# Kernel optimization log

Measured on AMD Instinct MI355X. Metric: run time of the kernel, lower is better.

The kernel has to match this reference:

```python
import jax, jax.numpy as jnp
import numpy as np


def setup_inputs() -> dict:
    key = jax.random.key(0)
    k1, k2, k3 = jax.random.split(key, 3)
    B, N, F_in, F_out = 8, 2048, 128, 128
    x = jax.random.normal(k1, (B, N, F_in), dtype=jnp.float32)
    adj = jax.random.uniform(k2, (B, N, N), dtype=jnp.float32)
    W = jax.random.normal(k3, (F_out, F_in), dtype=jnp.float32) * (1.0 / np.sqrt(F_in))
    b = jnp.zeros((F_out,), dtype=jnp.float32)
    return {"x": x, "adj": adj, "W": W, "b": b}


def reference(x, adj, W, b):
    # adj: [B,N,N], x: [B,N,F]
    N = adj.shape[-1]
    adj = adj + jnp.eye(N, dtype=adj.dtype)  # add self-loops
    d_inv_sqrt = jnp.sum(adj, axis=-1) ** -0.5  # [B,N]
    # D^-1/2 A D^-1/2 as row/col broadcast scale (same math as diag bmm)
    adj_norm = d_inv_sqrt[:, :, None] * adj * d_inv_sqrt[:, None, :]
    out = jnp.einsum('bnm,bmf->bnf', adj_norm, x)  # aggregate
    out = jnp.einsum('bnf,of->bno', out, W) + b    # linear
    return out
```

## Files before the change

kernel.cpp:

```cpp
#include <hip/hip_runtime.h>
#include <hip/hip_bf16.h>

typedef __attribute__((ext_vector_type(8))) short s16x8;
typedef __attribute__((ext_vector_type(4))) float f32x4;

#define B_  8
#define N_  2048
#define F_  128
#define BM  64
#define BK  64

__device__ __forceinline__ short bfc(float f) {
  __hip_bfloat16 h = __float2bfloat16(f);
  return __builtin_bit_cast(short, h);
}

__global__ __launch_bounds__(256) void k_deg(const float* __restrict__ adj,
                                             float* __restrict__ dinv) {
  const int row  = blockIdx.x * 4 + (threadIdx.x >> 6);
  const int lane = threadIdx.x & 63;
  const float* p = adj + (size_t)row * N_;
  float s = 0.f;
#pragma unroll
  for (int it = 0; it < 8; ++it) {
    float4 v = *reinterpret_cast<const float4*>(p + it * 256 + lane * 4);
    s += (v.x + v.y) + (v.z + v.w);
  }
#pragma unroll
  for (int off = 32; off > 0; off >>= 1) s += __shfl_down(s, off);
  if (lane == 0) dinv[row] = 1.0f / sqrtf(s + 1.0f);
}

__global__ __launch_bounds__(512) void k_gcn(const float* __restrict__ adj,
                                             const float* __restrict__ x,
                                             const float* __restrict__ W,
                                             const float* __restrict__ bias,
                                             const float* __restrict__ dinv,
                                             float* __restrict__ out) {
  __shared__ short s_mem[BM * 72 + F_ * 72];
  __shared__ short s_w[F_ * 136];
  short* const s_adj = s_mem;
  short* const s_xb  = s_mem + BM * 72;
  short* const s_o1  = s_mem;

  const int tid  = threadIdx.x;
  const int lane = tid & 63;
  const int wv   = tid >> 6;
  const int wrow = wv & 3;
  const int whal = wv >> 2;

  const int batch = blockIdx.x & 7;
  const int n0    = (blockIdx.x >> 3) * BM;

  {
    const int o  = tid >> 2;
    const int f0 = (tid & 3) * 32;
    const float* wp = W + o * F_ + f0;
#pragma unroll
    for (int u = 0; u < 8; ++u) {
      float4 v = *reinterpret_cast<const float4*>(wp + u * 4);
      short4 h;
      h.x = bfc(v.x); h.y = bfc(v.y); h.z = bfc(v.z); h.w = bfc(v.w);
      *reinterpret_cast<short4*>(&s_w[o * 136 + f0 + u * 4]) = h;
    }
  }

  const int ai  = tid >> 3;
  const int aj  = (tid & 7) * 8;
  const int xk2 = tid >> 4;
  const int xf0 = (tid & 15) * 8;

  const float* adj_row = adj + (size_t)(batch * N_ + n0 + ai) * N_;
  const float* x_b     = x + (size_t)batch * N_ * F_;
  const float* dv_b    = dinv + batch * N_;

  float4 ra0, ra1, rx0, rx1, rx2, rx3;
  float rd0, rd1;

  auto issue = [&](int k0) {
    ra0 = *reinterpret_cast<const float4*>(adj_row + k0 + aj);
    ra1 = *reinterpret_cast<const float4*>(adj_row + k0 + aj + 4);
    const float* xr = x_b + (size_t)(k0 + 2 * xk2) * F_ + xf0;
    rx0 = *reinterpret_cast<const float4*>(xr);
    rx1 = *reinterpret_cast<const float4*>(xr + 4);
    rx2 = *reinterpret_cast<const float4*>(xr + F_);
    rx3 = *reinterpret_cast<const float4*>(xr + F_ + 4);
    rd0 = dv_b[k0 + 2 * xk2];
    rd1 = dv_b[k0 + 2 * xk2 + 1];
  };

  f32x4 acc[4] = {};

  issue(0);
#pragma unroll 1
  for (int t = 0; t < N_ / BK; ++t) {
    __syncthreads();
    {
      s16x8 h;
      h[0] = bfc(ra0.x); h[1] = bfc(ra0.y); h[2] = bfc(ra0.z); h[3] = bfc(ra0.w);
      h[4] = bfc(ra1.x); h[5] = bfc(ra1.y); h[6] = bfc(ra1.z); h[7] = bfc(ra1.w);
      *reinterpret_cast<s16x8*>(&s_adj[ai * 72 + aj]) = h;
    }
    {
      float a0[8] = {rx0.x, rx0.y, rx0.z, rx0.w, rx1.x, rx1.y, rx1.z, rx1.w};
      float a1[8] = {rx2.x, rx2.y, rx2.z, rx2.w, rx3.x, rx3.y, rx3.z, rx3.w};
      const int kbase = (2 * xk2) ^ ((tid & 7) << 3);
#pragma unroll
      for (int u = 0; u < 8; ++u) {
        unsigned lo = (unsigned short)bfc(a0[u] * rd0);
        unsigned hi = (unsigned short)bfc(a1[u] * rd1);
        *reinterpret_cast<unsigned*>(&s_xb[(xf0 + u) * 72 + kbase]) = lo | (hi << 16);
      }
    }
    if (t + 1 < N_ / BK) issue((t + 1) * BK);
    __syncthreads();
    {
      const int arow = (wrow * 16 + (lane & 15)) * 72 + ((lane >> 4) * 8);
      s16x8 a0 = *reinterpret_cast<const s16x8*>(&s_adj[arow]);
      s16x8 a1 = *reinterpret_cast<const s16x8*>(&s_adj[arow + 32]);
      const int krun = (lane >> 4) * 8;
#pragma unroll
      for (int ct = 0; ct < 4; ++ct) {
        const int f   = whal * 64 + ct * 16 + (lane & 15);
        const int xsw = ((f >> 3) & 7) << 3;
        s16x8 b0 = *reinterpret_cast<const s16x8*>(&s_xb[f * 72 + (krun ^ xsw)]);
        s16x8 b1 = *reinterpret_cast<const s16x8*>(&s_xb[f * 72 + ((krun + 32) ^ xsw)]);
        acc[ct] = __builtin_amdgcn_mfma_f32_16x16x32_bf16(a0, b0, acc[ct], 0, 0, 0);
        acc[ct] = __builtin_amdgcn_mfma_f32_16x16x32_bf16(a1, b1, acc[ct], 0, 0, 0);
      }
    }
  }

  __syncthreads();
  {
    const int lr4 = (lane >> 4) * 4;
    const int lc  = lane & 15;
#pragma unroll
    for (int r = 0; r < 4; ++r) {
      const int nl = wrow * 16 + lr4 + r;
      const float dn = dv_b[n0 + nl];
      const float* xrow = x_b + (size_t)(n0 + nl) * F_;
#pragma unroll
      for (int ct = 0; ct < 4; ++ct) {
        const int f = whal * 64 + ct * 16 + lc;
        const float val = dn * acc[ct][r] + dn * dn * xrow[f];
        s_o1[nl * 136 + f] = bfc(val);
      }
    }
  }
  __syncthreads();

  f32x4 acc2[4] = {};
  {
    const int lc   = lane & 15;
    const int krun = (lane >> 4) * 8;
#pragma unroll
    for (int kk = 0; kk < 4; ++kk) {
      s16x8 af = *reinterpret_cast<const s16x8*>(
          &s_o1[(wrow * 16 + lc) * 136 + kk * 32 + krun]);
#pragma unroll
      for (int ot = 0; ot < 4; ++ot) {
        const int o = whal * 64 + ot * 16 + lc;
        s16x8 bf8 = *reinterpret_cast<const s16x8*>(&s_w[o * 136 + kk * 32 + krun]);
        acc2[ot] = __builtin_amdgcn_mfma_f32_16x16x32_bf16(af, bf8, acc2[ot], 0, 0, 0);
      }
    }
  }
  {
    const int lr4 = (lane >> 4) * 4;
    const int lc  = lane & 15;
#pragma unroll
    for (int ot = 0; ot < 4; ++ot) {
      const int o  = whal * 64 + ot * 16 + lc;
      const float bb = bias[o];
#pragma unroll
      for (int r = 0; r < 4; ++r) {
        const int nl = wrow * 16 + lr4 + r;
        out[(size_t)(batch * N_ + n0 + nl) * F_ + o] = acc2[ot][r] + bb;
      }
    }
  }
}

extern "C" void kernel_launch(void* const* d_in, const int* in_sizes, int n_in,
                              void* d_out, int out_size, void* d_ws, size_t ws_size,
                              hipStream_t stream) {
  const float* x   = (const float*)d_in[0];
  const float* adj = (const float*)d_in[1];
  const float* W   = (const float*)d_in[2];
  const float* b   = (const float*)d_in[3];
  float* outp  = (float*)d_out;
  float* dinv  = (float*)d_ws;

  k_deg<<<(B_ * N_) / 4, 256, 0, stream>>>(adj, dinv);
  k_gcn<<<B_ * (N_ / BM), 512, 0, stream>>>(adj, x, W, b, dinv, outp);
}
```

Baseline: 60.51 us.

## Pre-pack scaled bf16 x tiles and double-buffer via direct global-to-LDS loads

Adds a prep kernel that scales x by dinv, converts it to bf16 and writes it pre-swizzled and transposed into workspace tiles. The main kernel then streams those tiles straight into LDS with global_load_lds into double buffers, prefetches adj two steps ahead, and halves the row tile to 32 so the grid has twice as many blocks for occupancy. This removes the per-block repeated conversion of x and the register staging, at the cost of an extra launch and workspace traffic. A fallback kernel keeps the old path when the workspace is too small.

```diff
diff --git a/kernel.cpp b/kernel.cpp
--- a/kernel.cpp
+++ b/kernel.cpp
@@ -7,12 +7,19 @@
 #define B_  8
 #define N_  2048
 #define F_  128
-#define BM  64
+#define BM  32
 #define BK  64
+#define NT  (N_/BK)
 
 __device__ __forceinline__ short bfc(float f) {
   __hip_bfloat16 h = __float2bfloat16(f);
   return __builtin_bit_cast(short, h);
+}
+
+__device__ __forceinline__ void gload16(const void* g, void* l) {
+  __builtin_amdgcn_global_load_lds(
+      (const __attribute__((address_space(1))) unsigned*)g,
+      (__attribute__((address_space(3))) unsigned*)l, 16, 0, 0);
 }
 
 __global__ __launch_bounds__(256) void k_deg(const float* __restrict__ adj,
@@ -31,16 +38,194 @@
   if (lane == 0) dinv[row] = 1.0f / sqrtf(s + 1.0f);
 }
 
-__global__ __launch_bounds__(512) void k_gcn(const float* __restrict__ adj,
-                                             const float* __restrict__ x,
-                                             const float* __restrict__ W,
-                                             const float* __restrict__ bias,
-                                             const float* __restrict__ dinv,
-                                             float* __restrict__ out) {
-  __shared__ short s_mem[BM * 72 + F_ * 72];
+__global__ __launch_bounds__(256) void k_prep(const float* __restrict__ x,
+                                              const float* __restrict__ dinv,
+                                              unsigned short* __restrict__ xt) {
+  __shared__ short s[F_ * 64];
+  const int b  = blockIdx.x >> 5;
+  const int t  = blockIdx.x & 31;
+  const int rp = threadIdx.x >> 3;
+  const int f0 = (threadIdx.x & 7) * 16;
+  const int r0 = rp * 2;
+  const float* x0 = x + ((size_t)(b * N_) + t * 64 + r0) * F_ + f0;
+  const float d0 = dinv[b * N_ + t * 64 + r0];
+  const float d1 = dinv[b * N_ + t * 64 + r0 + 1];
+#pragma unroll
+  for (int u = 0; u < 16; u += 4) {
+    float4 v0 = *reinterpret_cast<const float4*>(x0 + u);
+    float4 v1 = *reinterpret_cast<const float4*>(x0 + F_ + u);
+    float a0[4] = {v0.x, v0.y, v0.z, v0.w};
+    float a1[4] = {v1.x, v1.y, v1.z, v1.w};
+#pragma unroll
+    for (int j = 0; j < 4; ++j) {
+      const int f = f0 + u + j;
+      unsigned lo = (unsigned short)bfc(a0[j] * d0);
+      unsigned hi = (unsigned short)bfc(a1[j] * d1);
+      *reinterpret_cast<unsigned*>(&s[f * 64 + (r0 ^ ((f & 7) << 3))]) = lo | (hi << 16);
+    }
+  }
+  __syncthreads();
+  const s16x8* sp = reinterpret_cast<const s16x8*>(s);
+  s16x8* op = reinterpret_cast<s16x8*>(xt + (size_t)blockIdx.x * 8192);
+#pragma unroll
+  for (int j = 0; j < 4; ++j) op[threadIdx.x * 4 + j] = sp[threadIdx.x * 4 + j];
+}
+
+__global__ __launch_bounds__(512, 4) void k_gcn(const float* __restrict__ adj,
+                                                const float* __restrict__ x,
+                                                const float* __restrict__ W,
+                                                const float* __restrict__ bias,
+                                                const float* __restrict__ dinv,
+                                                const unsigned short* __restrict__ xt,
+                                                float* __restrict__ out) {
+  __shared__ short s_main[2 * BM * 64 + 2 * F_ * 64];
+  __shared__ short s_w[F_ * 136];
+  short* const sadj0 = s_main;
+  short* const sadj1 = s_main + 2048;
+  short* const sxt0  = s_main + 4096;
+  short* const sxt1  = s_main + 12288;
+  short* const s_o1  = s_main;
+
+  const int tid  = threadIdx.x;
+  const int lane = tid & 63;
+  const int wv   = tid >> 6;
+  const int wrow = wv & 1;
+  const int wcol = wv >> 1;
+
+  const int batch = blockIdx.x & 7;
+  const int n0    = (blockIdx.x >> 3) * BM;
+
+  {
+    const int o   = tid >> 2;
+    const int f0c = (tid & 3) * 32;
+    const float* wp = W + o * F_ + f0c;
+#pragma unroll
+    for (int u = 0; u < 8; ++u) {
+      float4 v = *reinterpret_cast<const float4*>(wp + u * 4);
+      short4 h;
+      h.x = bfc(v.x); h.y = bfc(v.y); h.z = bfc(v.z); h.w = bfc(v.w);
+      *reinterpret_cast<short4*>(&s_w[o * 136 + f0c + u * 4]) = h;
+    }
+  }
+  asm volatile("s_waitcnt vmcnt(0)" ::: "memory");
+  __builtin_amdgcn_sched_barrier(0);
+
+  const int ai = tid >> 4;
+  const int aj = (tid & 15) * 4;
+  const float* adj_row = adj + (size_t)(batch * N_ + n0 + ai) * N_ + aj;
+  const int a_lds = ai * 64 + (aj ^ ((ai & 7) << 3));
+
+  const unsigned short* xt_b = xt + (size_t)batch * NT * 8192;
+
+  f32x4 acc[2] = {};
+  float4 aA, aB;
+
+  aA = *reinterpret_cast<const float4*>(adj_row);
+  gload16(xt_b + tid * 8, sxt0 + tid * 8);
+  gload16(xt_b + 4096 + tid * 8, sxt0 + 4096 + tid * 8);
+  aB = *reinterpret_cast<const float4*>(adj_row + BK);
+
+  auto step = [&](int t, float4& aCur, short* sadj_c, short* sxt_c, short* sxt_n) {
+    {
+      short4 h;
+      h.x = bfc(aCur.x); h.y = bfc(aCur.y); h.z = bfc(aCur.z); h.w = bfc(aCur.w);
+      *reinterpret_cast<short4*>(&sadj_c[a_lds]) = h;
+    }
+    if (t < NT - 1) asm volatile("s_waitcnt vmcnt(1) lgkmcnt(0)" ::: "memory");
+    else            asm volatile("s_waitcnt vmcnt(0) lgkmcnt(0)" ::: "memory");
+    __builtin_amdgcn_s_barrier();
+    __builtin_amdgcn_sched_barrier(0);
+    if (t + 1 < NT) {
+      const unsigned short* src = xt_b + (size_t)(t + 1) * 8192;
+      gload16(src + tid * 8, sxt_n + tid * 8);
+      gload16(src + 4096 + tid * 8, sxt_n + 4096 + tid * 8);
+      if (t + 2 < NT) aCur = *reinterpret_cast<const float4*>(adj_row + (t + 2) * BK);
+    }
+    {
+      const int row  = wrow * 16 + (lane & 15);
+      const int swzr = (row & 7) << 3;
+      const int krun = (lane >> 4) * 8;
+      const short* sa = sadj_c + row * 64;
+      s16x8 a0 = *reinterpret_cast<const s16x8*>(sa + (krun ^ swzr));
+      s16x8 a1 = *reinterpret_cast<const s16x8*>(sa + ((32 + krun) ^ swzr));
+#pragma unroll
+      for (int ct = 0; ct < 2; ++ct) {
+        const int f    = wcol * 32 + ct * 16 + (lane & 15);
+        const int swzf = (f & 7) << 3;
+        const short* sb = sxt_c + f * 64;
+        s16x8 b0 = *reinterpret_cast<const s16x8*>(sb + (krun ^ swzf));
+        s16x8 b1 = *reinterpret_cast<const s16x8*>(sb + ((32 + krun) ^ swzf));
+        acc[ct] = __builtin_amdgcn_mfma_f32_16x16x32_bf16(a0, b0, acc[ct], 0, 0, 0);
+        acc[ct] = __builtin_amdgcn_mfma_f32_16x16x32_bf16(a1, b1, acc[ct], 0, 0, 0);
+      }
+    }
+  };
+
+#pragma unroll 1
+  for (int tt = 0; tt < NT; tt += 2) {
+    step(tt,     aA, sadj0, sxt0, sxt1);
+    step(tt + 1, aB, sadj1, sxt1, sxt0);
+  }
+
+  __syncthreads();
+  {
+    const int lr4 = (lane >> 4) * 4;
+    const int lc  = lane & 15;
+#pragma unroll
+    for (int r = 0; r < 4; ++r) {
+      const int nl = wrow * 16 + lr4 + r;
+      const float dn = dinv[batch * N_ + n0 + nl];
+      const float* xrow = x + (size_t)(batch * N_ + n0 + nl) * F_;
+#pragma unroll
+      for (int ct = 0; ct < 2; ++ct) {
+        const int f = wcol * 32 + ct * 16 + lc;
+        s_o1[nl * 136 + f] = bfc(dn * acc[ct][r] + dn * dn * xrow[f]);
+      }
+    }
+  }
+  __syncthreads();
+
+  f32x4 acc2[2] = {};
+  {
+    const int lc   = lane & 15;
+    const int krun = (lane >> 4) * 8;
+#pragma unroll
+    for (int kk = 0; kk < 4; ++kk) {
+      s16x8 af = *reinterpret_cast<const s16x8*>(&s_o1[(wrow * 16 + lc) * 136 + kk * 32 + krun]);
+#pragma unroll
+      for (int ot = 0; ot < 2; ++ot) {
+        const int o = wcol * 32 + ot * 16 + lc;
+        s16x8 bw = *reinterpret_cast<const s16x8*>(&s_w[o * 136 + kk * 32 + krun]);
+        acc2[ot] = __builtin_amdgcn_mfma_f32_16x16x32_bf16(af, bw, acc2[ot], 0, 0, 0);
+      }
+    }
+  }
+  {
+    const int lr4 = (lane >> 4) * 4;
+    const int lc  = lane & 15;
+#pragma unroll
+    for (int ot = 0; ot < 2; ++ot) {
+      const int o  = wcol * 32 + ot * 16 + lc;
+      const float bb = bias[o];
+#pragma unroll
+      for (int r = 0; r < 4; ++r) {
+        const int nl = wrow * 16 + lr4 + r;
+        out[(size_t)(batch * N_ + n0 + nl) * F_ + o] = acc2[ot][r] + bb;
+      }
+    }
+  }
+}
+
+__global__ __launch_bounds__(512) void k_gcn_fb(const float* __restrict__ adj,
+                                                const float* __restrict__ x,
+                                                const float* __restrict__ W,
+                                                const float* __restrict__ bias,
+                                                const float* __restrict__ dinv,
+                                                float* __restrict__ out) {
+  __shared__ short s_mem[64 * 72 + F_ * 72];
   __shared__ short s_w[F_ * 136];
   short* const s_adj = s_mem;
-  short* const s_xb  = s_mem + BM * 72;
+  short* const s_xb  = s_mem + 64 * 72;
   short* const s_o1  = s_mem;
 
   const int tid  = threadIdx.x;
@@ -50,7 +235,7 @@
   const int whal = wv >> 2;
 
   const int batch = blockIdx.x & 7;
-  const int n0    = (blockIdx.x >> 3) * BM;
+  const int n0    = (blockIdx.x >> 3) * 64;
 
   {
     const int o  = tid >> 2;
@@ -90,10 +275,9 @@
   };
 
   f32x4 acc[4] = {};
-
   issue(0);
 #pragma unroll 1
-  for (int t = 0; t < N_ / BK; ++t) {
+  for (int t = 0; t < N_ / 64; ++t) {
     __syncthreads();
     {
       s16x8 h;
@@ -112,7 +296,7 @@
         *reinterpret_cast<unsigned*>(&s_xb[(xf0 + u) * 72 + kbase]) = lo | (hi << 16);
       }
     }
-    if (t + 1 < N_ / BK) issue((t + 1) * BK);
+    if (t + 1 < N_ / 64) issue((t + 1) * 64);
     __syncthreads();
     {
       const int arow = (wrow * 16 + (lane & 15)) * 72 + ((lane >> 4) * 8);
@@ -143,8 +327,7 @@
 #pragma unroll
       for (int ct = 0; ct < 4; ++ct) {
         const int f = whal * 64 + ct * 16 + lc;
-        const float val = dn * acc[ct][r] + dn * dn * xrow[f];
-        s_o1[nl * 136 + f] = bfc(val);
+        s_o1[nl * 136 + f] = bfc(dn * acc[ct][r] + dn * dn * xrow[f]);
       }
     }
   }
@@ -156,8 +339,7 @@
     const int krun = (lane >> 4) * 8;
 #pragma unroll
     for (int kk = 0; kk < 4; ++kk) {
-      s16x8 af = *reinterpret_cast<const s16x8*>(
-          &s_o1[(wrow * 16 + lc) * 136 + kk * 32 + krun]);
+      s16x8 af = *reinterpret_cast<const s16x8*>(&s_o1[(wrow * 16 + lc) * 136 + kk * 32 + krun]);
 #pragma unroll
       for (int ot = 0; ot < 4; ++ot) {
         const int o = whal * 64 + ot * 16 + lc;
@@ -189,9 +371,15 @@
   const float* adj = (const float*)d_in[1];
   const float* W   = (const float*)d_in[2];
   const float* b   = (const float*)d_in[3];
-  float* outp  = (float*)d_out;
-  float* dinv  = (float*)d_ws;
+  float* outp = (float*)d_out;
+  float* dinv = (float*)d_ws;
+  unsigned short* xt = (unsigned short*)((char*)d_ws + 65536);
 
   k_deg<<<(B_ * N_) / 4, 256, 0, stream>>>(adj, dinv);
-  k_gcn<<<B_ * (N_ / BM), 512, 0, stream>>>(adj, x, W, b, dinv, outp);
-}
+  if (ws_size >= 65536 + (size_t)B_ * NT * 8192 * 2) {
+    k_prep<<<B_ * NT, 256, 0, stream>>>(x, dinv, xt);
+    k_gcn<<<B_ * (N_ / BM), 512, 0, stream>>>(adj, x, W, b, dinv, xt, outp);
+  } else {
+    k_gcn_fb<<<B_ * (N_ / 64), 512, 0, stream>>>(adj, x, W, b, dinv, outp);
+  }
+}
```

Result: faster. 58.24 us (-3.8%).
